# Kernel tuning notes

Measured on AMD Instinct MI355X. Metric: run time of the kernel, lower is better.

## Reference

```python
import jax, jax.numpy as jnp
import numpy as np

DIM = 1024
NUM_HEADS = 16
HEAD_DIM = DIM // NUM_HEADS
MLP_DIM = 4 * DIM
EPS = 1e-5


def layer_norm(x, g, b):
    mu = jnp.mean(x, axis=-1, keepdims=True)
    var = jnp.mean(jnp.square(x - mu), axis=-1, keepdims=True)
    return (x - mu) * jax.lax.rsqrt(var + EPS) * g + b


def setup_inputs() -> dict:
    key = jax.random.key(0)
    ks = jax.random.split(key, 12)
    B, L = 2, 2048
    s = lambda n: 1.0 / np.sqrt(n)
    return {
        "x": jax.random.normal(ks[0], (B, L, DIM), jnp.float32),
        "attn_mask": jnp.tril(jnp.ones((L, L), jnp.int32))[None, None],  # [1,1,L,L]
        "w_qkv": jax.random.normal(ks[1], (DIM, 3 * DIM), jnp.float32) * s(DIM),
        "b_qkv": jnp.zeros((3 * DIM,), jnp.float32),
        "w_proj": jax.random.normal(ks[2], (DIM, DIM), jnp.float32) * s(DIM),
        "b_proj": jnp.zeros((DIM,), jnp.float32),
        "w_fc1": jax.random.normal(ks[3], (DIM, MLP_DIM), jnp.float32) * s(DIM),
        "b_fc1": jnp.zeros((MLP_DIM,), jnp.float32),
        "w_fc2": jax.random.normal(ks[4], (MLP_DIM, DIM), jnp.float32) * s(MLP_DIM),
        "b_fc2": jnp.zeros((DIM,), jnp.float32),
        "g1": jnp.ones((DIM,), jnp.float32),
        "beta1": jnp.zeros((DIM,), jnp.float32),
        "g2": jnp.ones((DIM,), jnp.float32),
        "beta2": jnp.zeros((DIM,), jnp.float32),
    }


def reference(x, attn_mask, w_qkv, b_qkv, w_proj, b_proj, w_fc1, b_fc1,
              w_fc2, b_fc2, g1, beta1, g2, beta2):
    B, L, D = x.shape
    scale = HEAD_DIM ** -0.5

    # --- attention branch (pre-norm) ---
    h = layer_norm(x, g1, beta1)
    qkv = h @ w_qkv + b_qkv                                  # [B,L,3D]
    qkv = qkv.reshape(B, L, 3, NUM_HEADS, HEAD_DIM)
    q = qkv[:, :, 0].transpose(0, 2, 1, 3)                   # [B,H,L,hd]
    k = qkv[:, :, 1].transpose(0, 2, 1, 3)
    v = qkv[:, :, 2].transpose(0, 2, 1, 3)
    attn = jnp.einsum('bhqd,bhkd->bhqk', q, k) * scale       # [B,H,L,L]
    attn = jnp.where(attn_mask == 0, -jnp.inf, attn)
    attn = jax.nn.softmax(attn, axis=-1)
    y = jnp.einsum('bhqk,bhkd->bhqd', attn, v)               # [B,H,L,hd]
    y = y.transpose(0, 2, 1, 3).reshape(B, L, D)
    y = y @ w_proj + b_proj
    x = x + y

    # --- MLP branch (pre-norm) ---
    h = layer_norm(x, g2, beta2)
    h = jax.nn.gelu(h @ w_fc1 + b_fc1, approximate=False)
    h = h @ w_fc2 + b_fc2
    return x + h
```

## Files before the change

### kernel.cpp

```cpp
#include <hip/hip_runtime.h>
#include <hip/hip_bf16.h>
#include <stdint.h>

typedef unsigned short u16;
typedef __attribute__((ext_vector_type(8))) short bf16x8;
typedef __attribute__((ext_vector_type(4))) short bf16x4;
typedef __attribute__((ext_vector_type(4))) float f32x4;
typedef __attribute__((ext_vector_type(16))) float f32x16;
typedef __attribute__((ext_vector_type(4))) unsigned short u16x4;

#define DEVI static __device__ __forceinline__

DEVI u16 f2bf(float f) {
    unsigned int u = __builtin_bit_cast(unsigned int, f);
    return (u16)((u + 0x7fffu + ((u >> 16) & 1u)) >> 16);
}

DEVI float bf2f(u16 v) { return __builtin_bit_cast(float, ((unsigned)v) << 16); }

DEVI float4 ldbf4(const u16* p, size_t idx4) {
    const u16x4 v = ((const u16x4*)p)[idx4];
    float4 o;
    o.x = bf2f(v[0]); o.y = bf2f(v[1]); o.z = bf2f(v[2]); o.w = bf2f(v[3]);
    return o;
}

DEVI float gelu_f(float v) {
    const float z = 1.5957691216f * (v + 0.044715f * v * v * v);
    return v / (1.0f + __expf(-z));
}

DEVI void async_copy16(const void* g, void* l) {
    __builtin_amdgcn_global_load_lds((const __attribute__((address_space(1))) void*)g,
                                     (__attribute__((address_space(3))) void*)l,
                                     16, 0, 0);
}

__global__ __launch_bounds__(256) void prep_kernel(const float* __restrict__ wq, u16* __restrict__ dq,
                                                   const float* __restrict__ wp, u16* __restrict__ dp,
                                                   const float* __restrict__ w1, u16* __restrict__ d1,
                                                   const float* __restrict__ w2, u16* __restrict__ d2,
                                                   const float* __restrict__ x,
                                                   const float* __restrict__ g1,
                                                   const float* __restrict__ be1,
                                                   u16* __restrict__ ln1out) {
    __shared__ float tile[32][33];
    __shared__ float red[8];
    const int id = blockIdx.x;
    const int t = threadIdx.x;
    if (id >= 12288) {
        const int row = id - 12288;
        const float4 v = ((const float4*)(x + (size_t)row * 1024))[t];
        float s  = v.x + v.y + v.z + v.w;
        float ss = v.x * v.x + v.y * v.y + v.z * v.z + v.w * v.w;
#pragma unroll
        for (int off = 32; off > 0; off >>= 1) {
            s  += __shfl_down(s, off);
            ss += __shfl_down(ss, off);
        }
        const int wv = t >> 6;
        if ((t & 63) == 0) { red[wv] = s; red[4 + wv] = ss; }
        __syncthreads();
        if (t == 0) {
            red[0] = red[0] + red[1] + red[2] + red[3];
            red[4] = red[4] + red[5] + red[6] + red[7];
        }
        __syncthreads();
        const float mean = red[0] * (1.0f / 1024.0f);
        const float var  = red[4] * (1.0f / 1024.0f) - mean * mean;
        const float rstd = rsqrtf(var + 1e-5f);
        const float4 gv = ((const float4*)g1)[t];
        const float4 bv = ((const float4*)be1)[t];
        u16x4 o;
        o[0] = f2bf((v.x - mean) * rstd * gv.x + bv.x);
        o[1] = f2bf((v.y - mean) * rstd * gv.y + bv.y);
        o[2] = f2bf((v.z - mean) * rstd * gv.z + bv.z);
        o[3] = f2bf((v.w - mean) * rstd * gv.w + bv.w);
        ((u16x4*)ln1out)[(size_t)row * 256 + t] = o;
        return;
    }
    const float* src; u16* dst; int K, N, k0, n0;
    if (id < 3072)      {               src = wq; dst = dq; K = 1024; N = 3072; k0 = (id & 31) << 5; n0 = (id >> 5) << 5; }
    else if (id < 4096) { int l = id - 3072; src = wp; dst = dp; K = 1024; N = 1024; k0 = (l & 31) << 5; n0 = (l >> 5) << 5; }
    else if (id < 8192) { int l = id - 4096; src = w1; dst = d1; K = 1024; N = 4096; k0 = (l & 31) << 5; n0 = (l >> 5) << 5; }
    else                { int l = id - 8192; src = w2; dst = d2; K = 4096; N = 1024; k0 = (l & 127) << 5; n0 = (l >> 7) << 5; }
    const int c = t & 31, r0 = t >> 5;
#pragma unroll
    for (int p = 0; p < 4; ++p) {
        const int r = r0 + p * 8;
        tile[r][c] = src[(size_t)(k0 + r) * N + n0 + c];
    }
    __syncthreads();
#pragma unroll
    for (int p = 0; p < 4; ++p) {
        const int r = r0 + p * 8;
        dst[(size_t)(n0 + r) * K + k0 + c] = f2bf(tile[c][r]);
    }
}

DEVI void stage64(const char* g, size_t ldb, char* lds0, int lane, int wv) {
    const int colsw = ((lane & 3) << 4) ^ (lane & 32);
    const int rl = lane >> 2;
#pragma unroll
    for (int i = 0; i < 4; ++i) {
        const int s = wv * 4 + i;
        const int kh = s >> 3, c = s & 7;
        async_copy16(g + (size_t)(c * 16 + rl) * ldb + kh * 64 + colsw,
                     lds0 + s * 1024);
    }
}

template <int EPI, int SPLITK>
__global__ __launch_bounds__(256, 4) void gemmv6(const u16* __restrict__ A,
                                                 const u16* __restrict__ Bt,
                                                 const float* __restrict__ bias,
                                                 void* __restrict__ out0,
                                                 void* __restrict__ out1,
                                                 void* __restrict__ out2,
                                                 int M, int N, int K) {
    __shared__ __align__(16) char As[16384];
    __shared__ __align__(16) char Bs[16384];
    const int tid = threadIdx.x;
    const int lane = tid & 63, wv = tid >> 6;
    const int wr = wv >> 1, wc = wv & 1;
    const int g = lane >> 4, qq = lane & 15;
    const int rdoff = qq * 64 + ((g * 16) ^ ((qq & 8) << 2));

    const int nwg = gridDim.x;
    int id = blockIdx.x;
    id = (id & 7) * (nwg >> 3) + (id >> 3);
    const int MT = M >> 7, NTn = N >> 7;
    const int slice = id / (MT * NTn);
    const int r2 = id % (MT * NTn);
    const int m0 = (r2 % MT) << 7;
    const int n0 = (r2 / MT) << 7;
    const int Ks = K / SPLITK;
    const int NT = Ks >> 6;
    const size_t ldb = (size_t)K * 2;

    const char* pa = (const char*)A + (size_t)m0 * ldb + (size_t)slice * Ks * 2;
    const char* pb = (const char*)Bt + (size_t)n0 * ldb + (size_t)slice * Ks * 2;

    f32x4 acc[4][4] = {};

    for (int t = 0; t < NT; ++t) {
        stage64(pa + (size_t)t * 128, ldb, As, lane, wv);
        stage64(pb + (size_t)t * 128, ldb, Bs, lane, wv);
        __syncthreads();
#pragma unroll
        for (int kh = 0; kh < 2; ++kh) {
            bf16x8 fa[4], fb[4];
#pragma unroll
            for (int fn = 0; fn < 4; ++fn)
                fb[fn] = *(const bf16x8*)(Bs + (kh * 8 + wc * 4 + fn) * 1024 + rdoff);
#pragma unroll
            for (int fm = 0; fm < 4; ++fm)
                fa[fm] = *(const bf16x8*)(As + (kh * 8 + wr * 4 + fm) * 1024 + rdoff);
#pragma unroll
            for (int fm = 0; fm < 4; ++fm)
#pragma unroll
                for (int fn = 0; fn < 4; ++fn)
                    acc[fm][fn] = __builtin_amdgcn_mfma_f32_16x16x32_bf16(fa[fm], fb[fn],
                                                                          acc[fm][fn], 0, 0, 0);
        }
        __syncthreads();
    }

#pragma unroll
    for (int fm = 0; fm < 4; ++fm) {
#pragma unroll
        for (int fn = 0; fn < 4; ++fn) {
            const int mrow = m0 + wr * 64 + fm * 16 + g * 4;
            const int ncol = n0 + wc * 64 + fn * 16 + qq;
            if constexpr (EPI == 0) {
                const float bs = bias[ncol];
                const int sec = ncol >> 10;
                const int hd_ = ncol & 1023;
                const int hh = hd_ >> 6, dd = hd_ & 63;
                if (sec == 2) {
                    const int b_ = mrow >> 11, l_ = mrow & 2047;
                    u16x4 pk;
#pragma unroll
                    for (int r = 0; r < 4; ++r) pk[r] = f2bf(acc[fm][fn][r] + bs);
                    *(u16x4*)((u16*)out2 + ((size_t)((b_ * 16 + hh) * 64 + dd)) * 2048 + l_) = pk;
                } else {
                    u16* dst = (sec == 0) ? (u16*)out0 : (u16*)out1;
                    const float sc = (sec == 0) ? 0.1803368801f : 1.0f;
#pragma unroll
                    for (int r = 0; r < 4; ++r) {
                        const int mr = mrow + r;
                        const int b_ = mr >> 11, l_ = mr & 2047;
                        dst[((size_t)((b_ * 16 + hh) * 2048 + l_)) * 64 + dd] =
                            f2bf((acc[fm][fn][r] + bs) * sc);
                    }
                }
            } else if constexpr (EPI == 2) {
                const float bs = bias[ncol];
                u16* dst = (u16*)out0;
#pragma unroll
                for (int r = 0; r < 4; ++r)
                    dst[(size_t)(mrow + r) * N + ncol] = f2bf(gelu_f(acc[fm][fn][r] + bs));
            } else {
                u16* dst = (u16*)out0 + (size_t)slice * M * N;
#pragma unroll
                for (int r = 0; r < 4; ++r)
                    dst[(size_t)(mrow + r) * N + ncol] = f2bf(acc[fm][fn][r]);
            }
        }
    }
}

template <int SPLIT>
__global__ __launch_bounds__(256) void reduceN_kernel(const u16* __restrict__ p,
                                                      const float* __restrict__ bias,
                                                      const float* __restrict__ res,
                                                      float* __restrict__ out,
                                                      int MN4, int N4) {
    const int i = blockIdx.x * 256 + threadIdx.x;
    float4 s = ldbf4(p, i);
#pragma unroll
    for (int s2 = 1; s2 < SPLIT; ++s2) {
        const float4 q = ldbf4(p, (size_t)s2 * MN4 + i);
        s.x += q.x; s.y += q.y; s.z += q.z; s.w += q.w;
    }
    const float4 r = ((const float4*)res)[i];
    const float4 bs = ((const float4*)bias)[i & (N4 - 1)];
    float4 o;
    o.x = s.x + r.x + bs.x;
    o.y = s.y + r.y + bs.y;
    o.z = s.z + r.z + bs.z;
    o.w = s.w + r.w + bs.w;
    ((float4*)out)[i] = o;
}

template <int SPLIT>
__global__ __launch_bounds__(256) void reduceLN_kernel(const u16* __restrict__ p,
                                                       const float* __restrict__ bias,
                                                       const float* __restrict__ res,
                                                       const float* __restrict__ gw,
                                                       const float* __restrict__ bw,
                                                       float* __restrict__ xout,
                                                       u16* __restrict__ lnout,
                                                       int MN4) {
    const int row = blockIdx.x;
    const int t = threadIdx.x;
    const int i = row * 256 + t;
    float4 s = ldbf4(p, i);
#pragma unroll
    for (int s2 = 1; s2 < SPLIT; ++s2) {
        const float4 q = ldbf4(p, (size_t)s2 * MN4 + i);
        s.x += q.x; s.y += q.y; s.z += q.z; s.w += q.w;
    }
    const float4 r = ((const float4*)res)[i];
    const float4 bs = ((const float4*)bias)[t];
    float4 o;
    o.x = s.x + r.x + bs.x;
    o.y = s.y + r.y + bs.y;
    o.z = s.z + r.z + bs.z;
    o.w = s.w + r.w + bs.w;
    ((float4*)xout)[i] = o;
    float sum  = o.x + o.y + o.z + o.w;
    float ssum = o.x * o.x + o.y * o.y + o.z * o.z + o.w * o.w;
#pragma unroll
    for (int off = 32; off > 0; off >>= 1) {
        sum  += __shfl_down(sum, off);
        ssum += __shfl_down(ssum, off);
    }
    __shared__ float red[8];
    const int wv = t >> 6;
    if ((t & 63) == 0) { red[wv] = sum; red[4 + wv] = ssum; }
    __syncthreads();
    if (t == 0) {
        red[0] = red[0] + red[1] + red[2] + red[3];
        red[4] = red[4] + red[5] + red[6] + red[7];
    }
    __syncthreads();
    const float mean = red[0] * (1.0f / 1024.0f);
    const float var  = red[4] * (1.0f / 1024.0f) - mean * mean;
    const float rstd = rsqrtf(var + 1e-5f);
    const float4 gv = ((const float4*)gw)[t];
    const float4 bv = ((const float4*)bw)[t];
    u16x4 ov;
    ov[0] = f2bf((o.x - mean) * rstd * gv.x + bv.x);
    ov[1] = f2bf((o.y - mean) * rstd * gv.y + bv.y);
    ov[2] = f2bf((o.z - mean) * rstd * gv.z + bv.z);
    ov[3] = f2bf((o.w - mean) * rstd * gv.w + bv.w);
    ((u16x4*)lnout)[(size_t)row * 256 + t] = ov;
}

DEVI void stage_kv1(const char* kbase, const char* vbase, int key0,
                    u16* ksm, u16* vsm, int wv, int lane) {
#pragma unroll
    for (int i = 0; i < 2; ++i) {
        const int c = wv + i * 4;
        const int off = c * 1024 + lane * 16;
        const int row = off >> 7;
        const int scol = (off & 127) ^ ((row & 7) << 4);
        async_copy16(kbase + (size_t)key0 * 128 + (size_t)row * 128 + scol,
                     (char*)ksm + c * 1024);
    }
#pragma unroll
    for (int i = 0; i < 2; ++i) {
        const int c = wv + i * 4;
        const int row = c * 8 + (lane >> 3);
        const int scol = ((lane & 7) * 16) ^ ((row & 7) << 4);
        async_copy16(vbase + (size_t)row * 4096 + (size_t)key0 * 2 + scol,
                     (char*)vsm + c * 1024);
    }
}

__global__ __launch_bounds__(256, 4) void attn32_seg(const u16* __restrict__ Q,
                                                     const u16* __restrict__ Kk,
                                                     const u16* __restrict__ Vt,
                                                     u16* __restrict__ opart,
                                                     float2* __restrict__ ml) {
    const int id = blockIdx.x;
    const int bh = id & 31;
    const int seg = (id >> 5) & 1;
    const int qb = 15 - (id >> 6);
    const int tid = threadIdx.x;
    const int wv = tid >> 6, lane = tid & 63;
    const int hi = lane >> 5, qc = lane & 31;

    __shared__ __align__(16) u16 Ksm[4096];
    __shared__ __align__(16) u16 Vsm[4096];
    __shared__ __align__(16) u16 Pl[4][32 * 36];

    const char* Kb = (const char*)(Kk + (size_t)bh * 2048 * 64);
    const char* Vb = (const char*)(Vt + (size_t)bh * 64 * 2048);
    u16* Pw = &Pl[wv][0];
    const u16* Pr = Pw + qc * 36;

    const int q0w = qb * 128 + wv * 32;
    const int qg = q0w + qc;
    const int nt_half = qb + 1;
    const int kt_begin = seg ? nt_half : 0;
    const int kt_end = seg ? (2 * qb + 2) : nt_half;
    const int ntw = min(kt_end, 2 * qb + (wv >> 1) + 1);

    bf16x8 qf[4];
    {
        const u16* Qp = Q + ((size_t)bh * 2048 + qg) * 64;
#pragma unroll
        for (int c = 0; c < 4; ++c)
            qf[c] = *(const bf16x8*)(Qp + c * 16 + hi * 8);
    }

    f32x16 oacc[2];
#pragma unroll
    for (int r = 0; r < 16; ++r) { oacc[0][r] = 0.0f; oacc[1][r] = 0.0f; }
    float m_run = -60000.0f, l_run = 0.0f;

    for (int kt = kt_begin; kt < kt_end; ++kt) {
        const int key0 = kt * 64;
        stage_kv1(Kb, Vb, key0, Ksm, Vsm, wv, lane);
        __syncthreads();
        if (kt < ntw) {
            f32x16 sacc[2];
#pragma unroll
            for (int r = 0; r < 16; ++r) { sacc[0][r] = 0.0f; sacc[1][r] = 0.0f; }
#pragma unroll
            for (int c = 0; c < 4; ++c) {
#pragma unroll
                for (int kb = 0; kb < 2; ++kb) {
                    const int kr = kb * 32 + qc;
                    const bf16x8 ak = *(const bf16x8*)((const char*)Ksm + kr * 128 +
                                          ((c * 32 + hi * 16) ^ ((kr & 7) << 4)));
                    sacc[kb] = __builtin_amdgcn_mfma_f32_32x32x16_bf16(ak, qf[c],
                                                                       sacc[kb], 0, 0, 0);
                }
            }
            float pmax = -1e30f;
            if (key0 + 63 > q0w) {
#pragma unroll
                for (int kb = 0; kb < 2; ++kb)
#pragma unroll
                    for (int r = 0; r < 16; ++r) {
                        const int key = key0 + kb * 32 + (r & 3) + 8 * (r >> 2) + 4 * hi;
                        float s = sacc[kb][r];
                        if (key > qg) s = -1e30f;
                        sacc[kb][r] = s;
                        pmax = fmaxf(pmax, s);
                    }
            } else {
#pragma unroll
                for (int kb = 0; kb < 2; ++kb)
#pragma unroll
                    for (int r = 0; r < 16; ++r) pmax = fmaxf(pmax, sacc[kb][r]);
            }
            pmax = fmaxf(pmax, __shfl_xor(pmax, 32));
            if (pmax > m_run + 11.0f) {
                const float alpha = __builtin_amdgcn_exp2f(m_run - pmax);
#pragma unroll
                for (int r = 0; r < 16; ++r) { oacc[0][r] *= alpha; oacc[1][r] *= alpha; }
                l_run *= alpha;
                m_run = pmax;
            }
            float lsum = 0.0f;
#pragma unroll
            for (int kb = 0; kb < 2; ++kb) {
#pragma unroll
                for (int j = 0; j < 4; ++j) {
                    u16x4 pk4;
#pragma unroll
                    for (int t = 0; t < 4; ++t) {
                        const float e = __builtin_amdgcn_exp2f(sacc[kb][j * 4 + t] - m_run);
                        lsum += e;
                        pk4[t] = f2bf(e);
                    }
                    *(u16x4*)(Pw + qc * 36 + j * 8 + 4 * hi) = pk4;
                }
#pragma unroll
                for (int s = 0; s < 2; ++s) {
                    const int c = kb * 2 + s;
                    const bf16x8 pf = *(const bf16x8*)(Pr + s * 16 + hi * 8);
#pragma unroll
                    for (int db = 0; db < 2; ++db) {
                        const int dr = db * 32 + qc;
                        const bf16x8 av = *(const bf16x8*)((const char*)Vsm + dr * 128 +
                                              ((c * 32 + hi * 16) ^ ((dr & 7) << 4)));
                        oacc[db] = __builtin_amdgcn_mfma_f32_32x32x16_bf16(av, pf,
                                                                           oacc[db], 0, 0, 0);
                    }
                }
            }
            lsum += __shfl_xor(lsum, 32);
            l_run += lsum;
        }
        __syncthreads();
    }

    const size_t row = (size_t)seg * 65536 + (size_t)bh * 2048 + qg;
    u16* op = opart + row * 64;
#pragma unroll
    for (int db = 0; db < 2; ++db)
#pragma unroll
        for (int j = 0; j < 4; ++j) {
            u16x4 o;
#pragma unroll
            for (int t = 0; t < 4; ++t) o[t] = f2bf(oacc[db][j * 4 + t]);
            *(u16x4*)(op + db * 32 + j * 8 + 4 * hi) = o;
        }
    if (hi == 0) { float2 t2; t2.x = m_run; t2.y = l_run; ml[row] = t2; }
}

__global__ __launch_bounds__(256) void attn_comb2(const u16* __restrict__ opart,
                                                  const float2* __restrict__ ml,
                                                  u16* __restrict__ Y) {
    const int idx = blockIdx.x * 256 + threadIdx.x;
    const int row = idx >> 4, d4 = idx & 15;
    const float2 ml0 = ml[row];
    const float2 ml1 = ml[65536 + row];
    const float m = fmaxf(ml0.x, ml1.x);
    const float w0 = __builtin_amdgcn_exp2f(ml0.x - m);
    const float w1 = __builtin_amdgcn_exp2f(ml1.x - m);
    const float inv = 1.0f / (ml0.y * w0 + ml1.y * w1);
    const float4 a = ldbf4(opart, (size_t)row * 16 + d4);
    const float4 b = ldbf4(opart, (size_t)(65536 + row) * 16 + d4);
    const int bh = row >> 11, q = row & 2047;
    const int b_ = bh >> 4, hh = bh & 15;
    u16x4 o;
    o[0] = f2bf((a.x * w0 + b.x * w1) * inv);
    o[1] = f2bf((a.y * w0 + b.y * w1) * inv);
    o[2] = f2bf((a.z * w0 + b.z * w1) * inv);
    o[3] = f2bf((a.w * w0 + b.w * w1) * inv);
    *(u16x4*)(Y + ((size_t)(b_ * 2048 + q)) * 1024 + hh * 64 + d4 * 4) = o;
}

extern "C" void kernel_launch(void* const* d_in, const int* in_sizes, int n_in,
                              void* d_out, int out_size, void* d_ws, size_t ws_size,
                              hipStream_t stream) {
    (void)in_sizes; (void)n_in; (void)out_size;
    const float* x      = (const float*)d_in[0];
    const float* w_qkv  = (const float*)d_in[2];
    const float* b_qkv  = (const float*)d_in[3];
    const float* w_proj = (const float*)d_in[4];
    const float* b_proj = (const float*)d_in[5];
    const float* w_fc1  = (const float*)d_in[6];
    const float* b_fc1  = (const float*)d_in[7];
    const float* w_fc2  = (const float*)d_in[8];
    const float* b_fc2  = (const float*)d_in[9];
    const float* g1     = (const float*)d_in[10];
    const float* be1    = (const float*)d_in[11];
    const float* g2     = (const float*)d_in[12];
    const float* be2    = (const float*)d_in[13];

    char* ws = (char*)d_ws;
    size_t off = 0;
    auto alloc = [&](size_t bytes) { size_t r = off; off += (bytes + 255) & ~(size_t)255; return r; };
    u16*   wt_qkv = (u16*)(ws + alloc((size_t)3072 * 1024 * 2));
    u16*   wt_prj = (u16*)(ws + alloc((size_t)1024 * 1024 * 2));
    u16*   wt_fc1 = (u16*)(ws + alloc((size_t)4096 * 1024 * 2));
    u16*   wt_fc2 = (u16*)(ws + alloc((size_t)1024 * 4096 * 2));
    u16*   hbuf   = (u16*)(ws + alloc((size_t)4096 * 1024 * 2));
    float* x1     = (float*)(ws + alloc((size_t)4096 * 1024 * 4));
    char*  big    = ws + alloc((size_t)33554432);
    u16* qb  = (u16*)(big);
    u16* kb  = (u16*)(big + 8388608);
    u16* vtb = (u16*)(big + 16777216);
    u16* yb  = (u16*)(big + 25165824);
    u16* act = (u16*)(big);
    if (off > ws_size) return;
    const size_t part_need = (size_t)4 * 4096 * 1024 * 2;
    if ((ws_size - off) < part_need) return;
    u16* part = (u16*)(ws + off);
    u16* opart = part;
    float2* mlp = (float2*)(ws + off + (size_t)2 * 65536 * 64 * 2);

    const dim3 blk(256);
    prep_kernel<<<dim3(16384), blk, 0, stream>>>(w_qkv, wt_qkv, w_proj, wt_prj,
                                                 w_fc1, wt_fc1, w_fc2, wt_fc2,
                                                 x, g1, be1, hbuf);
    gemmv6<0, 1><<<dim3(768), blk, 0, stream>>>(hbuf, wt_qkv, b_qkv,
                                                qb, kb, vtb, 4096, 3072, 1024);
    attn32_seg<<<dim3(1024), blk, 0, stream>>>(qb, kb, vtb, opart, mlp);
    attn_comb2<<<dim3(4096), blk, 0, stream>>>(opart, mlp, yb);
    gemmv6<5, 2><<<dim3(512), blk, 0, stream>>>(yb, wt_prj, nullptr,
                                                part, nullptr, nullptr, 4096, 1024, 1024);
    reduceLN_kernel<2><<<dim3(4096), blk, 0, stream>>>(part, b_proj, x, g2, be2,
                                                       x1, hbuf, 1048576);
    gemmv6<2, 1><<<dim3(1024), blk, 0, stream>>>(hbuf, wt_fc1, b_fc1,
                                                 act, nullptr, nullptr, 4096, 4096, 1024);
    gemmv6<5, 4><<<dim3(1024), blk, 0, stream>>>(act, wt_fc2, nullptr,
                                                 part, nullptr, nullptr, 4096, 1024, 4096);
    reduceN_kernel<4><<<dim3(4096), blk, 0, stream>>>(part, b_fc2, x1, (float*)d_out,
                                                      1048576, 256);
}
```

Measured before the change: 221.1 us.

## Add 256x256 eight-wave GEMM with quad-buffered LDS pipeline for MLP GEMMs

Introduces a new gemm8 kernel that uses 512-thread blocks, 256x256 output tiles and four A/B LDS buffers of 16 KB each. Global-to-LDS async copies of later K-tiles are interleaved with MFMA phases, and setprio is raised around the MFMA blocks. The kernel replaces the previous gemmv6 for the fc1 and fc2 GEMMs, aiming for more data reuse and better overlap of loads with compute. The cost is 128 KB of LDS and one block per CU, with 256 blocks in the grid. Correctness depends on the hand-placed waitcnt and barrier ordering.

```diff
diff --git a/kernel.cpp b/kernel.cpp
--- a/kernel.cpp
+++ b/kernel.cpp
@@ -194,7 +194,131 @@
                             f2bf((acc[fm][fn][r] + bs) * sc);
                     }
                 }
-            } else if constexpr (EPI == 2) {
+            } else {
+                u16* dst = (u16*)out0 + (size_t)slice * M * N;
+#pragma unroll
+                for (int r = 0; r < 4; ++r)
+                    dst[(size_t)(mrow + r) * N + ncol] = f2bf(acc[fm][fn][r]);
+            }
+        }
+    }
+}
+
+DEVI void stage_half8(const char* g, size_t ldb, char* lds0, int lane, int wv) {
+    const int colsw = ((lane & 3) << 4) ^ (lane & 32);
+    const int rl = lane >> 2;
+#pragma unroll
+    for (int i = 0; i < 2; ++i) {
+        const int c = wv + i * 8;
+        async_copy16(g + (size_t)(c * 16 + rl) * ldb + colsw, lds0 + c * 1024);
+    }
+}
+
+template <int EPI, int SPLITK>
+__global__ __launch_bounds__(512, 1) void gemm8(const u16* __restrict__ A,
+                                                const u16* __restrict__ Bt,
+                                                const float* __restrict__ bias,
+                                                void* __restrict__ out0,
+                                                int M, int N, int K) {
+    __shared__ __align__(16) char A00[16384];
+    __shared__ __align__(16) char A01[16384];
+    __shared__ __align__(16) char A10[16384];
+    __shared__ __align__(16) char A11[16384];
+    __shared__ __align__(16) char B00[16384];
+    __shared__ __align__(16) char B01[16384];
+    __shared__ __align__(16) char B10[16384];
+    __shared__ __align__(16) char B11[16384];
+    const int tid = threadIdx.x;
+    const int lane = tid & 63, wv = tid >> 6;
+    const int wr = wv >> 2, wc = wv & 3;
+    const int g = lane >> 4, qq = lane & 15;
+    const int rdoff = qq * 64 + ((g * 16) ^ ((qq & 8) << 2));
+
+    int id = blockIdx.x;
+    id = (id & 7) * (gridDim.x >> 3) + (id >> 3);
+    const int MT = M >> 8, NTn = N >> 8;
+    const int slice = id / (MT * NTn);
+    const int r2 = id % (MT * NTn);
+    const int m0 = (r2 % MT) << 8;
+    const int n0 = (r2 / MT) << 8;
+    const int Ks = K / SPLITK;
+    const int NT = Ks >> 6;
+    const size_t ldb = (size_t)K * 2;
+
+    const char* pa = (const char*)A + (size_t)m0 * ldb + (size_t)slice * Ks * 2;
+    const char* pb = (const char*)Bt + (size_t)n0 * ldb + (size_t)slice * Ks * 2;
+
+    f32x4 acc[8][4] = {};
+    bf16x8 fb[4];
+
+    auto dophase = [&](const char* Aks, const char* Bks, int MH,
+                       const char* sg, char* sl) {
+        if (MH == 0) {
+#pragma unroll
+            for (int fn = 0; fn < 4; ++fn)
+                fb[fn] = *(const bf16x8*)(Bks + (wc * 4 + fn) * 1024 + rdoff);
+        }
+        bf16x8 fa[4];
+#pragma unroll
+        for (int i2 = 0; i2 < 4; ++i2)
+            fa[i2] = *(const bf16x8*)(Aks + (wr * 8 + MH * 4 + i2) * 1024 + rdoff);
+        stage_half8(sg, ldb, sl, lane, wv);
+        __builtin_amdgcn_s_barrier();
+        asm volatile("s_waitcnt lgkmcnt(0)" ::: "memory");
+        __builtin_amdgcn_sched_barrier(0);
+        __builtin_amdgcn_s_setprio(1);
+#pragma unroll
+        for (int fn = 0; fn < 4; ++fn)
+#pragma unroll
+            for (int i2 = 0; i2 < 4; ++i2)
+                acc[MH * 4 + i2][fn] = __builtin_amdgcn_mfma_f32_16x16x32_bf16(
+                    fa[i2], fb[fn], acc[MH * 4 + i2][fn], 0, 0, 0);
+        __builtin_amdgcn_s_setprio(0);
+        __builtin_amdgcn_sched_barrier(0);
+    };
+
+    stage_half8(pa,       ldb, A00, lane, wv);
+    stage_half8(pb,       ldb, B00, lane, wv);
+    stage_half8(pa + 64,  ldb, A01, lane, wv);
+    stage_half8(pb + 64,  ldb, B01, lane, wv);
+    stage_half8(pa + 128, ldb, A10, lane, wv);
+    stage_half8(pb + 128, ldb, B10, lane, wv);
+    asm volatile("s_waitcnt vmcnt(4)" ::: "memory");
+    __builtin_amdgcn_s_barrier();
+
+    const int NI = NT >> 1;
+    for (int i = 0; i < NI; ++i) {
+        const size_t t1o = (size_t)(2 * i + 1) * 128;
+        const size_t t2o = (size_t)((2 * i + 2 < NT) ? 2 * i + 2 : NT - 1) * 128;
+        const size_t t3o = (size_t)((2 * i + 3 < NT) ? 2 * i + 3 : NT - 1) * 128;
+
+        dophase(A00, B00, 0, pa + t1o + 64, A11);
+        __builtin_amdgcn_s_barrier();
+        dophase(A00, B00, 1, pb + t1o + 64, B11);
+        __builtin_amdgcn_s_barrier();
+        dophase(A01, B01, 0, pa + t2o,      A00);
+        __builtin_amdgcn_s_barrier();
+        dophase(A01, B01, 1, pb + t2o,      B00);
+        asm volatile("s_waitcnt vmcnt(4)" ::: "memory");
+        __builtin_amdgcn_s_barrier();
+        dophase(A10, B10, 0, pa + t2o + 64, A01);
+        __builtin_amdgcn_s_barrier();
+        dophase(A10, B10, 1, pb + t2o + 64, B01);
+        __builtin_amdgcn_s_barrier();
+        dophase(A11, B11, 0, pa + t3o,      A10);
+        __builtin_amdgcn_s_barrier();
+        dophase(A11, B11, 1, pb + t3o,      B10);
+        asm volatile("s_waitcnt vmcnt(4)" ::: "memory");
+        __builtin_amdgcn_s_barrier();
+    }
+
+#pragma unroll
+    for (int fm = 0; fm < 8; ++fm) {
+#pragma unroll
+        for (int fn = 0; fn < 4; ++fn) {
+            const int mrow = m0 + wr * 128 + fm * 16 + g * 4;
+            const int ncol = n0 + wc * 64 + fn * 16 + qq;
+            if constexpr (EPI == 2) {
                 const float bs = bias[ncol];
                 u16* dst = (u16*)out0;
 #pragma unroll
@@ -519,10 +643,10 @@
                                                 part, nullptr, nullptr, 4096, 1024, 1024);
     reduceLN_kernel<2><<<dim3(4096), blk, 0, stream>>>(part, b_proj, x, g2, be2,
                                                        x1, hbuf, 1048576);
-    gemmv6<2, 1><<<dim3(1024), blk, 0, stream>>>(hbuf, wt_fc1, b_fc1,
-                                                 act, nullptr, nullptr, 4096, 4096, 1024);
-    gemmv6<5, 4><<<dim3(1024), blk, 0, stream>>>(act, wt_fc2, nullptr,
-                                                 part, nullptr, nullptr, 4096, 1024, 4096);
+    gemm8<2, 1><<<dim3(256), dim3(512), 0, stream>>>(hbuf, wt_fc1, b_fc1,
+                                                     act, 4096, 4096, 1024);
+    gemm8<5, 4><<<dim3(256), dim3(512), 0, stream>>>(act, wt_fc2, nullptr,
+                                                     part, 4096, 1024, 4096);
     reduceN_kernel<4><<<dim3(4096), blk, 0, stream>>>(part, b_fc2, x1, (float*)d_out,
                                                       1048576, 256);
 }
```

Result: no change. 224.9 us (+1.7%).
